# Kernel tuning notes

Measured on AMD Instinct MI355X. Metric: run time of the kernel, lower is better.

The kernel has to match this reference:

```python
import jax, jax.numpy as jnp
import numpy as np

B, N, F_IN, H, E = 8, 10000, 128, 128, 160000


def setup_inputs() -> dict:
    key = jax.random.key(0)
    ks = jax.random.split(key, 6)
    x = jax.random.normal(ks[0], (B, N, F_IN), dtype=jnp.float32)
    edge_index = jax.random.randint(ks[1], (2, E), 0, N, dtype=jnp.int64)
    # GCNConv params (glorot-ish scale), LayerNorm affine params
    W1 = jax.random.normal(ks[2], (F_IN, H), dtype=jnp.float32) / np.sqrt(F_IN)
    b1 = jnp.zeros((H,), dtype=jnp.float32)
    W2 = jax.random.normal(ks[3], (H, H), dtype=jnp.float32) / np.sqrt(H)
    b2 = jnp.zeros((H,), dtype=jnp.float32)
    ln_w = jnp.ones((H,), dtype=jnp.float32)
    ln_b = jnp.zeros((H,), dtype=jnp.float32)
    return {"x": x, "edge_index": edge_index, "W1": W1, "b1": b1,
            "W2": W2, "b2": b2, "ln_w": ln_w, "ln_b": ln_b}


def reference(x, edge_index, W1, b1, W2, b2, ln_w, ln_b):
    # x: [B, N, F]; edge_index: [2, E] shared across batch (tiled per graph
    # in the original via node offsets -> equivalent to vmapping over batch).
    n = x.shape[1]
    loops = jnp.arange(n, dtype=edge_index.dtype)
    src = jnp.concatenate([edge_index[0], loops])  # add self-loops (GCNConv default)
    dst = jnp.concatenate([edge_index[1], loops])
    # symmetric degree normalization: deg over targets with self-loops
    deg = jax.ops.segment_sum(jnp.ones(dst.shape[0], dtype=x.dtype), dst, num_segments=n)
    dinv = jnp.where(deg > 0, jax.lax.rsqrt(deg), 0.0)
    w_e = dinv[src] * dinv[dst]  # [E+N] per-edge norm

    def gcn_agg(h):  # h: [B, N, H] -> gather, scale, scatter-add
        msg = h[:, src, :] * w_e[None, :, None]  # [B, E+N, H]
        return jax.vmap(lambda m: jax.ops.segment_sum(m, dst, num_segments=n))(msg)

    h1 = jax.nn.relu(gcn_agg(x @ W1) + b1)
    h2 = gcn_agg(h1 @ W2) + b2
    # LayerNorm over last dim (eps=1e-5, torch default)
    mu = jnp.mean(h2, axis=-1, keepdims=True)
    var = jnp.mean(jnp.square(h2 - mu), axis=-1, keepdims=True)
    out = (h2 - mu) * jax.lax.rsqrt(var + 1e-5) * ln_w + ln_b
    return out  # [B, N, H]
```

## Files before the change

kernel.cpp:

```cpp
#include <hip/hip_runtime.h>
#include <hip/hip_bf16.h>

#define NNODES 10000
#define NB 8
#define NF 128
#define NE 160000

typedef __attribute__((ext_vector_type(8))) short  short8;
typedef __attribute__((ext_vector_type(8))) unsigned short ushort8;
typedef __attribute__((ext_vector_type(4))) float  f32x4;

__device__ __forceinline__ unsigned short f2b(float f) {
    union { float f; unsigned u; } v; v.f = f;
    unsigned r = v.u + 0x7FFF + ((v.u >> 16) & 1);
    return (unsigned short)(r >> 16);
}
__device__ __forceinline__ unsigned int f2b2(float a, float b) {
    union { __hip_bfloat162 h; unsigned int u; } v;
    v.h = __float22bfloat162_rn(make_float2(a, b));
    return v.u;
}
__device__ __forceinline__ float b2f_lo(unsigned u) {
    union { unsigned u; float f; } v; v.u = u << 16; return v.f;
}
__device__ __forceinline__ float b2f_hi(unsigned u) {
    union { unsigned u; float f; } v; v.u = u & 0xffff0000u; return v.f;
}


__global__ void k_zero(int* __restrict__ cnt, int* __restrict__ fill) {
    int i = blockIdx.x * blockDim.x + threadIdx.x;
    if (i < NNODES) cnt[i] = 0;
    else if (i < 2 * NNODES) fill[i - NNODES] = 0;
}

__global__ void k_count(const int* __restrict__ ei, int* __restrict__ cnt) {
    int e = blockIdx.x * blockDim.x + threadIdx.x;
    if (e < NE) atomicAdd(&cnt[ei[NE + e]], 1);
}

__global__ void k_scan(const int* __restrict__ cnt, int* __restrict__ row_ptr,
                       float* __restrict__ dinv) {
    __shared__ int part[1024];
    int t = threadIdx.x;
    const int CH = (NNODES + 1023) / 1024;
    int lo = t * CH, hi = min(lo + CH, NNODES);
    int s = 0;
    for (int i = lo; i < hi; i++) {
        int c = cnt[i];
        dinv[i] = rsqrtf((float)(c + 1));
        s += c;
    }
    part[t] = s;
    __syncthreads();
    for (int off = 1; off < 1024; off <<= 1) {
        int v = (t >= off) ? part[t - off] : 0;
        __syncthreads();
        part[t] += v;
        __syncthreads();
    }
    int base = part[t] - s;
    for (int i = lo; i < hi; i++) { row_ptr[i] = base; base += cnt[i]; }
    if (t == 1023) row_ptr[NNODES] = part[1023];
}

__global__ void k_scatter(const int* __restrict__ ei, const int* __restrict__ row_ptr,
                          int* __restrict__ fill, const float* __restrict__ dinv,
                          uint2* __restrict__ edge) {
    int e = blockIdx.x * blockDim.x + threadIdx.x;
    if (e >= NE) return;
    int s = ei[e];
    int d = ei[NE + e];
    int pos = row_ptr[d] + atomicAdd(&fill[d], 1);
    edge[pos] = make_uint2((unsigned)s, __float_as_uint(dinv[s] * dinv[d]));
}

__global__ void k_wt2(const float* __restrict__ W1, unsigned short* __restrict__ Wt1,
                      const float* __restrict__ W2, unsigned short* __restrict__ Wt2) {
    int bid = blockIdx.x;
    const float* W = (bid < 64) ? W1 : W2;
    unsigned short* Wt = (bid < 64) ? Wt1 : Wt2;
    int id = (bid & 63) * 256 + threadIdx.x;
    int n = id >> 7, k = id & 127;
    Wt[(size_t)n * 128 + k] = f2b(W[(size_t)k * 128 + n]);
}

template <bool ABF16>
__global__ __launch_bounds__(256) void k_mm_mfma(const void* __restrict__ Ap,
                                                 const unsigned short* __restrict__ Wt,
                                                 unsigned short* __restrict__ Cn) {
    __shared__ unsigned short wlds[128 * 136];
    const int t = threadIdx.x;
    {
        const int r = t >> 1, h = t & 1;
        const ushort8* src = (const ushort8*)(Wt + r * 128 + h * 64);
        #pragma unroll
        for (int i = 0; i < 8; i++)
            *(ushort8*)(wlds + r * 136 + h * 64 + i * 8) = src[i];
    }
    __syncthreads();

    const int wid = t >> 6, lane = t & 63;
    const int quad = lane >> 4, l16 = lane & 15;
    const int m0 = blockIdx.x * 128 + (wid & 1) * 64;
    const int nb = (wid >> 1) * 64;
    const int kq = quad * 8;

    f32x4 acc[4][4] = {};

    #pragma unroll
    for (int ks = 0; ks < 128; ks += 32) {
        short8 bf[4];
        #pragma unroll
        for (int mi = 0; mi < 4; mi++) {
            const size_t row = (size_t)(m0 + mi * 16 + l16);
            if constexpr (ABF16) {
                bf[mi] = *(const short8*)((const unsigned short*)Ap + row * 128 + ks + kq);
            } else {
                const float* p = (const float*)Ap + row * 128 + ks + kq;
                float4 u0 = *(const float4*)p;
                float4 u1 = *(const float4*)(p + 4);
                union { uint4 u4; short8 s8; } cv;
                cv.u4.x = f2b2(u0.x, u0.y); cv.u4.y = f2b2(u0.z, u0.w);
                cv.u4.z = f2b2(u1.x, u1.y); cv.u4.w = f2b2(u1.z, u1.w);
                bf[mi] = cv.s8;
            }
        }
        short8 af[4];
        #pragma unroll
        for (int ni = 0; ni < 4; ni++)
            af[ni] = *(const short8*)(wlds + (nb + ni * 16 + l16) * 136 + ks + kq);
        #pragma unroll
        for (int mi = 0; mi < 4; mi++)
            #pragma unroll
            for (int ni = 0; ni < 4; ni++)
                acc[mi][ni] = __builtin_amdgcn_mfma_f32_16x16x32_bf16(
                    af[ni], bf[mi], acc[mi][ni], 0, 0, 0);
    }

    __syncthreads();
    {
        const int rbase = (wid & 1) * 64;
        #pragma unroll
        for (int mi = 0; mi < 4; mi++) {
            int rr = rbase + mi * 16 + l16;
            #pragma unroll
            for (int ni = 0; ni < 4; ni++) {
                uint2 p;
                p.x = f2b2(acc[mi][ni][0], acc[mi][ni][1]);
                p.y = f2b2(acc[mi][ni][2], acc[mi][ni][3]);
                *(uint2*)(wlds + rr * 136 + nb + ni * 16 + quad * 4) = p;
            }
        }
    }
    __syncthreads();
    {
        const int r = t >> 1, h = t & 1;
        int gm = blockIdx.x * 128 + r;
        int b = gm / NNODES;
        int n = gm - b * NNODES;
        unsigned short* dst = Cn + ((size_t)n * NB + b) * 128 + h * 64;
        const unsigned short* srow = wlds + r * 136 + h * 64;
        #pragma unroll
        for (int i = 0; i < 8; i++)
            *(ushort8*)(dst + i * 8) = *(const ushort8*)(srow + i * 8);
    }
}


__global__ __launch_bounds__(256) void k_agg_relu(const unsigned int* __restrict__ hNu,
                                                  const float* __restrict__ bias,
                                                  const int* __restrict__ row_ptr,
                                                  const uint2* __restrict__ edge,
                                                  const float* __restrict__ dinv,
                                                  unsigned int* __restrict__ h1u) {
    const int t = threadIdx.x;
    const int b = blockIdx.x & 7;
    const int g = blockIdx.x >> 3;
    const int wid = __builtin_amdgcn_readfirstlane(t >> 6);
    const int lane = t & 63;
    const int n = g * 4 + wid;

    const unsigned int* base = hNu + (size_t)b * 64 + lane;
    float di = dinv[n];
    float wself = di * di;
    unsigned int u = base[(size_t)n * 512];
    float a0 = b2f_lo(u) * wself;
    float a1 = b2f_hi(u) * wself;

    int e = row_ptr[n], e1 = row_ptr[n + 1];
    for (; e + 8 <= e1; e += 8) {
        uint2 E[8];
        #pragma unroll
        for (int j = 0; j < 8; j++) E[j] = edge[e + j];
        unsigned int U[8];
        #pragma unroll
        for (int j = 0; j < 8; j++) U[j] = base[(size_t)E[j].x * 512];
        #pragma unroll
        for (int j = 0; j < 8; j++) {
            float w = __uint_as_float(E[j].y);
            a0 = fmaf(b2f_lo(U[j]), w, a0);
            a1 = fmaf(b2f_hi(U[j]), w, a1);
        }
    }
    for (; e + 4 <= e1; e += 4) {
        uint2 E[4];
        #pragma unroll
        for (int j = 0; j < 4; j++) E[j] = edge[e + j];
        unsigned int U[4];
        #pragma unroll
        for (int j = 0; j < 4; j++) U[j] = base[(size_t)E[j].x * 512];
        #pragma unroll
        for (int j = 0; j < 4; j++) {
            float w = __uint_as_float(E[j].y);
            a0 = fmaf(b2f_lo(U[j]), w, a0);
            a1 = fmaf(b2f_hi(U[j]), w, a1);
        }
    }
    for (; e < e1; ++e) {
        uint2 E = edge[e];
        float w = __uint_as_float(E.y);
        unsigned int uu = base[(size_t)E.x * 512];
        a0 = fmaf(b2f_lo(uu), w, a0);
        a1 = fmaf(b2f_hi(uu), w, a1);
    }
    a0 = fmaxf(a0 + bias[lane * 2], 0.f);
    a1 = fmaxf(a1 + bias[lane * 2 + 1], 0.f);
    __builtin_nontemporal_store(f2b2(a0, a1), &h1u[((size_t)b * NNODES + n) * 64 + lane]);
}

__global__ __launch_bounds__(256) void k_agg_ln(const unsigned int* __restrict__ hNu,
                                                const float* __restrict__ bias,
                                                const int* __restrict__ row_ptr,
                                                const uint2* __restrict__ edge,
                                                const float* __restrict__ dinv,
                                                const float* __restrict__ ln_w,
                                                const float* __restrict__ ln_b,
                                                float* __restrict__ out) {
    const int t = threadIdx.x;
    const int b = blockIdx.x & 7;
    const int g = blockIdx.x >> 3;
    const int wid = __builtin_amdgcn_readfirstlane(t >> 6);
    const int lane = t & 63;
    const int n = g * 4 + wid;

    const unsigned int* base = hNu + (size_t)b * 64 + lane;
    float di = dinv[n];
    float wself = di * di;
    unsigned int u = base[(size_t)n * 512];
    float a0 = b2f_lo(u) * wself;
    float a1 = b2f_hi(u) * wself;

    int e = row_ptr[n], e1 = row_ptr[n + 1];
    for (; e + 8 <= e1; e += 8) {
        uint2 E[8];
        #pragma unroll
        for (int j = 0; j < 8; j++) E[j] = edge[e + j];
        unsigned int U[8];
        #pragma unroll
        for (int j = 0; j < 8; j++) U[j] = base[(size_t)E[j].x * 512];
        #pragma unroll
        for (int j = 0; j < 8; j++) {
            float w = __uint_as_float(E[j].y);
            a0 = fmaf(b2f_lo(U[j]), w, a0);
            a1 = fmaf(b2f_hi(U[j]), w, a1);
        }
    }
    for (; e + 4 <= e1; e += 4) {
        uint2 E[4];
        #pragma unroll
        for (int j = 0; j < 4; j++) E[j] = edge[e + j];
        unsigned int U[4];
        #pragma unroll
        for (int j = 0; j < 4; j++) U[j] = base[(size_t)E[j].x * 512];
        #pragma unroll
        for (int j = 0; j < 4; j++) {
            float w = __uint_as_float(E[j].y);
            a0 = fmaf(b2f_lo(U[j]), w, a0);
            a1 = fmaf(b2f_hi(U[j]), w, a1);
        }
    }
    for (; e < e1; ++e) {
        uint2 E = edge[e];
        float w = __uint_as_float(E.y);
        unsigned int uu = base[(size_t)E.x * 512];
        a0 = fmaf(b2f_lo(uu), w, a0);
        a1 = fmaf(b2f_hi(uu), w, a1);
    }
    a0 += bias[lane * 2];
    a1 += bias[lane * 2 + 1];

    float s1 = a0 + a1;
    float s2 = a0 * a0 + a1 * a1;
    #pragma unroll
    for (int m = 1; m < 64; m <<= 1) {
        s1 += __shfl_xor(s1, m);
        s2 += __shfl_xor(s2, m);
    }
    float mu = s1 * (1.f / NF);
    float var = s2 * (1.f / NF) - mu * mu;
    float rs = rsqrtf(var + 1e-5f);

    float o0 = (a0 - mu) * rs * ln_w[lane * 2] + ln_b[lane * 2];
    float o1 = (a1 - mu) * rs * ln_w[lane * 2 + 1] + ln_b[lane * 2 + 1];
    float* dst = out + ((size_t)b * NNODES + n) * 128 + lane * 2;
    __builtin_nontemporal_store(o0, dst);
    __builtin_nontemporal_store(o1, dst + 1);
}


extern "C" void kernel_launch(void* const* d_in, const int* in_sizes, int n_in,
                              void* d_out, int out_size, void* d_ws, size_t ws_size,
                              hipStream_t stream) {
    const float* x    = (const float*)d_in[0];
    const int*   ei   = (const int*)d_in[1];
    const float* W1   = (const float*)d_in[2];
    const float* b1   = (const float*)d_in[3];
    const float* W2   = (const float*)d_in[4];
    const float* b2   = (const float*)d_in[5];
    const float* ln_w = (const float*)d_in[6];
    const float* ln_b = (const float*)d_in[7];
    float* out = (float*)d_out;

    char* ws = (char*)d_ws;
    int*            cnt     = (int*)(ws + 0);
    int*            fill    = (int*)(ws + 40192);
    int*            row_ptr = (int*)(ws + 80384);
    float*          dinv    = (float*)(ws + 120832);
    uint2*          edge    = (uint2*)(ws + 161024);
    unsigned short* hA16    = (unsigned short*)(ws + 1441024);
    unsigned short* h1b     = (unsigned short*)(ws + 21921024);
    unsigned short* Wt1     = (unsigned short*)cnt;
    unsigned short* Wt2     = (unsigned short*)fill;

    k_zero   <<<(2 * NNODES + 255) / 256, 256, 0, stream>>>(cnt, fill);
    k_count  <<<(NE + 255) / 256, 256, 0, stream>>>(ei, cnt);
    k_scan   <<<1, 1024, 0, stream>>>(cnt, row_ptr, dinv);
    k_scatter<<<(NE + 255) / 256, 256, 0, stream>>>(ei, row_ptr, fill, dinv, edge);
    k_wt2    <<<128, 256, 0, stream>>>(W1, Wt1, W2, Wt2);

    k_mm_mfma<false><<<(NB * NNODES) / 128, 256, 0, stream>>>(x, Wt1, hA16);
    k_agg_relu<<<(NNODES / 4) * NB, 256, 0, stream>>>((const unsigned int*)hA16, b1,
                                                      row_ptr, edge, dinv,
                                                      (unsigned int*)h1b);

    k_mm_mfma<true><<<(NB * NNODES) / 128, 256, 0, stream>>>(h1b, Wt2, hA16);
    k_agg_ln<<<(NNODES / 4) * NB, 256, 0, stream>>>((const unsigned int*)hA16, b2,
                                                    row_ptr, edge, dinv,
                                                    ln_w, ln_b, out);
}
```

Measured before the change: 231.6 us.

## Pack edges into 32-bit words and switch feature layout to batch-major

Edge records shrink from 8 bytes to 4 by packing a 16-bit source index with a bf16 normalization weight, halving edge-list traffic in both aggregation kernels. The matmul output is now stored batch-major ([B,N,H]) instead of node-major interleaved ([N,B,H]), so each aggregation block's gathers hit a contiguous per-graph slab of about 2.5 MB. Together these aim to reduce memory traffic and improve cache locality in the gather-bound aggregation. The trade-off is that edge weights lose precision to bf16, and the 16-bit source index relies on N being below 65536.

```diff
diff --git a/kernel.cpp b/kernel.cpp
--- a/kernel.cpp
+++ b/kernel.cpp
@@ -66,13 +66,13 @@
 
 __global__ void k_scatter(const int* __restrict__ ei, const int* __restrict__ row_ptr,
                           int* __restrict__ fill, const float* __restrict__ dinv,
-                          uint2* __restrict__ edge) {
+                          unsigned int* __restrict__ edge) {
     int e = blockIdx.x * blockDim.x + threadIdx.x;
     if (e >= NE) return;
     int s = ei[e];
     int d = ei[NE + e];
     int pos = row_ptr[d] + atomicAdd(&fill[d], 1);
-    edge[pos] = make_uint2((unsigned)s, __float_as_uint(dinv[s] * dinv[d]));
+    edge[pos] = (unsigned)s | ((unsigned)f2b(dinv[s] * dinv[d]) << 16);
 }
 
 __global__ void k_wt2(const float* __restrict__ W1, unsigned short* __restrict__ Wt1,
@@ -156,10 +156,8 @@
     __syncthreads();
     {
         const int r = t >> 1, h = t & 1;
-        int gm = blockIdx.x * 128 + r;
-        int b = gm / NNODES;
-        int n = gm - b * NNODES;
-        unsigned short* dst = Cn + ((size_t)n * NB + b) * 128 + h * 64;
+        size_t gm = (size_t)blockIdx.x * 128 + r;
+        unsigned short* dst = Cn + gm * 128 + h * 64;
         const unsigned short* srow = wlds + r * 136 + h * 64;
         #pragma unroll
         for (int i = 0; i < 8; i++)
@@ -171,7 +169,7 @@
 __global__ __launch_bounds__(256) void k_agg_relu(const unsigned int* __restrict__ hNu,
                                                   const float* __restrict__ bias,
                                                   const int* __restrict__ row_ptr,
-                                                  const uint2* __restrict__ edge,
+                                                  const unsigned int* __restrict__ edge,
                                                   const float* __restrict__ dinv,
                                                   unsigned int* __restrict__ h1u) {
     const int t = threadIdx.x;
@@ -181,46 +179,46 @@
     const int lane = t & 63;
     const int n = g * 4 + wid;
 
-    const unsigned int* base = hNu + (size_t)b * 64 + lane;
+    const unsigned int* base = hNu + (size_t)b * NNODES * 64 + lane;
     float di = dinv[n];
     float wself = di * di;
-    unsigned int u = base[(size_t)n * 512];
+    unsigned int u = base[(size_t)n * 64];
     float a0 = b2f_lo(u) * wself;
     float a1 = b2f_hi(u) * wself;
 
     int e = row_ptr[n], e1 = row_ptr[n + 1];
     for (; e + 8 <= e1; e += 8) {
-        uint2 E[8];
+        unsigned int E[8];
         #pragma unroll
         for (int j = 0; j < 8; j++) E[j] = edge[e + j];
         unsigned int U[8];
         #pragma unroll
-        for (int j = 0; j < 8; j++) U[j] = base[(size_t)E[j].x * 512];
+        for (int j = 0; j < 8; j++) U[j] = base[(size_t)(E[j] & 0xffffu) * 64];
         #pragma unroll
         for (int j = 0; j < 8; j++) {
-            float w = __uint_as_float(E[j].y);
+            float w = b2f_hi(E[j]);
             a0 = fmaf(b2f_lo(U[j]), w, a0);
             a1 = fmaf(b2f_hi(U[j]), w, a1);
         }
     }
     for (; e + 4 <= e1; e += 4) {
-        uint2 E[4];
+        unsigned int E[4];
         #pragma unroll
         for (int j = 0; j < 4; j++) E[j] = edge[e + j];
         unsigned int U[4];
         #pragma unroll
-        for (int j = 0; j < 4; j++) U[j] = base[(size_t)E[j].x * 512];
+        for (int j = 0; j < 4; j++) U[j] = base[(size_t)(E[j] & 0xffffu) * 64];
         #pragma unroll
         for (int j = 0; j < 4; j++) {
-            float w = __uint_as_float(E[j].y);
+            float w = b2f_hi(E[j]);
             a0 = fmaf(b2f_lo(U[j]), w, a0);
             a1 = fmaf(b2f_hi(U[j]), w, a1);
         }
     }
     for (; e < e1; ++e) {
-        uint2 E = edge[e];
-        float w = __uint_as_float(E.y);
-        unsigned int uu = base[(size_t)E.x * 512];
+        unsigned int E = edge[e];
+        float w = b2f_hi(E);
+        unsigned int uu = base[(size_t)(E & 0xffffu) * 64];
         a0 = fmaf(b2f_lo(uu), w, a0);
         a1 = fmaf(b2f_hi(uu), w, a1);
     }
@@ -232,7 +230,7 @@
 __global__ __launch_bounds__(256) void k_agg_ln(const unsigned int* __restrict__ hNu,
                                                 const float* __restrict__ bias,
                                                 const int* __restrict__ row_ptr,
-                                                const uint2* __restrict__ edge,
+                                                const unsigned int* __restrict__ edge,
                                                 const float* __restrict__ dinv,
                                                 const float* __restrict__ ln_w,
                                                 const float* __restrict__ ln_b,
@@ -244,46 +242,46 @@
     const int lane = t & 63;
     const int n = g * 4 + wid;
 
-    const unsigned int* base = hNu + (size_t)b * 64 + lane;
+    const unsigned int* base = hNu + (size_t)b * NNODES * 64 + lane;
     float di = dinv[n];
     float wself = di * di;
-    unsigned int u = base[(size_t)n * 512];
+    unsigned int u = base[(size_t)n * 64];
     float a0 = b2f_lo(u) * wself;
     float a1 = b2f_hi(u) * wself;
 
     int e = row_ptr[n], e1 = row_ptr[n + 1];
     for (; e + 8 <= e1; e += 8) {
-        uint2 E[8];
+        unsigned int E[8];
         #pragma unroll
         for (int j = 0; j < 8; j++) E[j] = edge[e + j];
         unsigned int U[8];
         #pragma unroll
-        for (int j = 0; j < 8; j++) U[j] = base[(size_t)E[j].x * 512];
+        for (int j = 0; j < 8; j++) U[j] = base[(size_t)(E[j] & 0xffffu) * 64];
         #pragma unroll
         for (int j = 0; j < 8; j++) {
-            float w = __uint_as_float(E[j].y);
+            float w = b2f_hi(E[j]);
             a0 = fmaf(b2f_lo(U[j]), w, a0);
             a1 = fmaf(b2f_hi(U[j]), w, a1);
         }
     }
     for (; e + 4 <= e1; e += 4) {
-        uint2 E[4];
+        unsigned int E[4];
         #pragma unroll
         for (int j = 0; j < 4; j++) E[j] = edge[e + j];
         unsigned int U[4];
         #pragma unroll
-        for (int j = 0; j < 4; j++) U[j] = base[(size_t)E[j].x * 512];
+        for (int j = 0; j < 4; j++) U[j] = base[(size_t)(E[j] & 0xffffu) * 64];
         #pragma unroll
         for (int j = 0; j < 4; j++) {
-            float w = __uint_as_float(E[j].y);
+            float w = b2f_hi(E[j]);
             a0 = fmaf(b2f_lo(U[j]), w, a0);
             a1 = fmaf(b2f_hi(U[j]), w, a1);
         }
     }
     for (; e < e1; ++e) {
-        uint2 E = edge[e];
-        float w = __uint_as_float(E.y);
-        unsigned int uu = base[(size_t)E.x * 512];
+        unsigned int E = edge[e];
+        float w = b2f_hi(E);
+        unsigned int uu = base[(size_t)(E & 0xffffu) * 64];
         a0 = fmaf(b2f_lo(uu), w, a0);
         a1 = fmaf(b2f_hi(uu), w, a1);
     }
@@ -327,7 +325,7 @@
     int*            fill    = (int*)(ws + 40192);
     int*            row_ptr = (int*)(ws + 80384);
     float*          dinv    = (float*)(ws + 120832);
-    uint2*          edge    = (uint2*)(ws + 161024);
+    unsigned int*   edge    = (unsigned int*)(ws + 161024);
     unsigned short* hA16    = (unsigned short*)(ws + 1441024);
     unsigned short* h1b     = (unsigned short*)(ws + 21921024);
     unsigned short* Wt1     = (unsigned short*)cnt;
```

Measured after the change: 230.0 us. Within noise of the previous version (-0.7%).
